# Optimization experiments

Measured on AMD Instinct MI355X. Metric: run time of the kernel, lower is better.

Reference implementation:

```python
import jax, jax.numpy as jnp
import numpy as np

N_NODES = 50000
N_EDGES = 1600000
IN_CH = 128
HID_CH = 128


def setup_inputs() -> dict:
    key = jax.random.key(0)
    ks = jax.random.split(key, 8)
    node_embed = jax.random.normal(ks[0], (N_NODES, IN_CH), dtype=jnp.float32)
    node_pos = jax.random.normal(ks[1], (N_NODES, 3), dtype=jnp.float32)
    edge_index = jax.random.randint(ks[2], (2, N_EDGES), 0, N_NODES, dtype=jnp.int64)
    # Linear weights stored as [in, out] so y = x @ W + b (matches torch x @ W.T + b)
    W_res = jax.random.normal(ks[3], (IN_CH, HID_CH), dtype=jnp.float32) / np.sqrt(IN_CH)
    W_msg = jax.random.normal(ks[4], (2 * IN_CH + 1, HID_CH), dtype=jnp.float32) / np.sqrt(2 * IN_CH + 1)
    b_msg = jax.random.normal(ks[5], (HID_CH,), dtype=jnp.float32) * 0.01
    W_upd = jax.random.normal(ks[6], (IN_CH + HID_CH, HID_CH), dtype=jnp.float32) / np.sqrt(IN_CH + HID_CH)
    b_upd = jax.random.normal(ks[7], (HID_CH,), dtype=jnp.float32) * 0.01
    return {"node_embed": node_embed, "node_pos": node_pos, "edge_index": edge_index,
            "W_res": W_res, "W_msg": W_msg, "b_msg": b_msg, "W_upd": W_upd, "b_upd": b_upd}


def reference(node_embed, node_pos, edge_index, W_res, W_msg, b_msg, W_upd, b_upd):
    row, col = edge_index[0], edge_index[1]
    # squared distance per edge: [E, 1]
    diff = node_pos[row] - node_pos[col]
    dist = jnp.sum(diff * diff, axis=1, keepdims=True)
    # message MLP on concat(src, tgt, dist): [E, 2*in+1] -> [E, hidden]
    msg_in = jnp.concatenate([node_embed[row], node_embed[col], dist], axis=-1)
    msg = jax.nn.relu(msg_in @ W_msg + b_msg)
    # scatter-sum messages into target nodes (index = col, as in original)
    aggr = jax.ops.segment_sum(msg, col, num_segments=N_NODES)
    upd_in = jnp.concatenate([node_embed, aggr], axis=-1)
    new_node_embed = node_embed @ W_res + jax.nn.relu(upd_in @ W_upd + b_upd)
    return new_node_embed
```

## Files before the change

### kernel.cpp

```cpp
#include <hip/hip_runtime.h>
#include <hip/hip_bf16.h>
#include <cstdint>


typedef __bf16 bf16x8 __attribute__((ext_vector_type(8)));
typedef float floatx4 __attribute__((ext_vector_type(4)));
typedef float floatx2 __attribute__((ext_vector_type(2)));
typedef unsigned int uintx4 __attribute__((ext_vector_type(4)));

#define NBINS 1024
#define BIN_CAP 2560
#define CAP_OUT 2816
#define CUR_STRIDE 32

__device__ __forceinline__ ushort f2bf(float f) {
  union { float f; uint i; } v; v.f = f;
  uint r = v.i + 0x7fff + ((v.i >> 16) & 1);
  return (ushort)(r >> 16);
}
__device__ __forceinline__ bf16x8 load_frag(const ushort* p) {
  uint4 v = *(const uint4*)p;
  return __builtin_bit_cast(bf16x8, v);
}
__device__ __forceinline__ floatx2 pmax0(floatx2 a) {
#if __has_builtin(__builtin_elementwise_max)
  return __builtin_elementwise_max(a, (floatx2)(0.f));
#else
  floatx2 r; r.x = fmaxf(a.x, 0.f); r.y = fmaxf(a.y, 0.f); return r;
#endif
}
__device__ __forceinline__ floatx2 cvtpk2(uint qu) {
#if __has_builtin(__builtin_amdgcn_cvt_pk_f32_fp8)
  return __builtin_amdgcn_cvt_pk_f32_fp8((int)qu, false);
#else
  floatx2 o = {__builtin_amdgcn_cvt_f32_fp8((int)qu, 0),
               __builtin_amdgcn_cvt_f32_fp8((int)qu, 1)};
  return o;
#endif
}

struct WSrc { const float* s[5]; };

__global__ __launch_bounds__(256) void k01_cast_bin(
    const float* __restrict__ embed, ushort* __restrict__ Eb, int n4, int nb_cast,
    WSrc ws, ushort* __restrict__ Wt,
    const int* __restrict__ ei, int E,
    uint* __restrict__ bin_cursor, uint* __restrict__ binned, int bb)
{
  __shared__ uint hist[NBINS];
  __shared__ uint sbase[NBINS];
  __shared__ uint lcur[NBINS];

  if ((int)blockIdx.x >= bb) {
    int cb = blockIdx.x - bb;
    if (cb < nb_cast) {
      int i = cb * 256 + threadIdx.x;
      if (i < n4) {
        float4 v = ((const float4*)embed)[i];
        ushort4 o;
        o.x = f2bf(v.x); o.y = f2bf(v.y); o.z = f2bf(v.z); o.w = f2bf(v.w);
        ((ushort4*)Eb)[i] = o;
      }
      return;
    }
    int wb = cb - nb_cast;
    const float* s = ws.s[wb];
    ushort* d = Wt + wb * 16384;
    for (int i = threadIdx.x; i < 16384; i += 256) {
      int k = i >> 7, n = i & 127;
      d[n * 128 + k] = f2bf(s[i]);
    }
    return;
  }

  const int t = threadIdx.x;
#pragma unroll
  for (int k = 0; k < NBINS / 256; ++k) hist[t + k * 256] = 0;
  __syncthreads();

  const int e0 = blockIdx.x * 2048 + t * 8;
  int rr[8], cc[8];
  bool any = (e0 < E);
  if (any) {
    int4 r0 = ((const int4*)(ei + e0))[0];
    int4 r1 = ((const int4*)(ei + e0))[1];
    int4 c0 = ((const int4*)(ei + E + e0))[0];
    int4 c1 = ((const int4*)(ei + E + e0))[1];
    rr[0]=r0.x; rr[1]=r0.y; rr[2]=r0.z; rr[3]=r0.w;
    rr[4]=r1.x; rr[5]=r1.y; rr[6]=r1.z; rr[7]=r1.w;
    cc[0]=c0.x; cc[1]=c0.y; cc[2]=c0.z; cc[3]=c0.w;
    cc[4]=c1.x; cc[5]=c1.y; cc[6]=c1.z; cc[7]=c1.w;
#pragma unroll
    for (int j = 0; j < 8; ++j) {
      if (e0 + j < E) atomicAdd(&hist[cc[j] >> 6], 1u);
    }
  }
  __syncthreads();
#pragma unroll
  for (int k = 0; k < NBINS / 256; ++k) {
    int b2 = t + k * 256;
    uint h = hist[b2];
    sbase[b2] = h ? atomicAdd(bin_cursor + b2 * CUR_STRIDE, h) : 0u;
    lcur[b2] = 0;
  }
  __syncthreads();
  if (any) {
#pragma unroll
    for (int j = 0; j < 8; ++j) {
      if (e0 + j < E) {
        int b = cc[j] >> 6;
        uint ofs = atomicAdd(&lcur[b], 1u);
        uint idx = sbase[b] + ofs;
        if (idx < BIN_CAP)
          binned[(size_t)b * BIN_CAP + idx] = ((uint)cc[j] << 16) | (uint)rr[j];
      }
    }
  }
}

__global__ __launch_bounds__(256) void k2_proj_sort(
    const ushort* __restrict__ Ab, int M, int rt,
    const ushort* __restrict__ W1t, const ushort* __restrict__ W2t,
    const float* __restrict__ b_msg, const float* __restrict__ pos,
    unsigned char* __restrict__ P1, ushort* __restrict__ P2b,
    const uint* __restrict__ bin_cursor, const uint* __restrict__ binned,
    uint* __restrict__ sorted, int* __restrict__ nstart, int* __restrict__ ncnt)
{
  __shared__ ushort sdist[BIN_CAP];
  __shared__ uint   srt[CAP_OUT];
  __shared__ float  spos[64 * 3];
  __shared__ uint   h[64], st[64], lc[64];
  __shared__ uint   stot;

  if ((int)blockIdx.x >= rt) {
    const int bin = blockIdx.x - rt;
    const int col0 = bin * 64;
    const int tid = threadIdx.x;
    const int cnt = (int)min(bin_cursor[bin * CUR_STRIDE], (uint)BIN_CAP);
    const uint* src = binned + (size_t)bin * BIN_CAP;
    const int ncol = min(64, M - col0);

    if (tid < 64) { h[tid] = 0; lc[tid] = 0; }
    for (int i = tid; i < ncol * 3; i += 256) spos[i] = pos[(size_t)col0 * 3 + i];
    __syncthreads();

    for (int i = tid; i < cnt; i += 256) {
      uint rc = src[i];
      uint row = rc & 0xffffu, cl = (rc >> 16) & 63u;
      float dx = spos[cl * 3 + 0] - pos[(size_t)row * 3 + 0];
      float dy = spos[cl * 3 + 1] - pos[(size_t)row * 3 + 1];
      float dz = spos[cl * 3 + 2] - pos[(size_t)row * 3 + 2];
      sdist[i] = f2bf(dx * dx + dy * dy + dz * dz);
      atomicAdd(&h[cl], 1u);
    }
    __syncthreads();

    if (tid == 0) {
      uint s = 0;
      for (int c = 0; c < 64; ++c) { st[c] = s; s += (h[c] + 3u) & ~3u; }
      stot = s;
    }
    __syncthreads();

    for (int i = tid; i < cnt; i += 256) {
      uint rc = src[i];
      uint row = rc & 0xffffu, cl = (rc >> 16) & 63u;
      uint p = st[cl] + atomicAdd(&lc[cl], 1u);
      if (p < CAP_OUT) srt[p] = (row << 16) | (uint)sdist[i];
    }
    __syncthreads();

    uint tot = min(stot, (uint)CAP_OUT);
    for (int i = tid; i < (int)tot; i += 256)
      sorted[(size_t)bin * CAP_OUT + i] = srt[i];
    if (tid < 64 && tid < ncol) {
      nstart[col0 + tid] = bin * CAP_OUT + (int)st[tid];
      ncnt[col0 + tid] = (int)h[tid];
    }
    return;
  }

  const int wv = threadIdx.x >> 6, lane = threadIdx.x & 63;
  const int q = lane >> 4, lr = lane & 15;
  const int m0 = blockIdx.x * 32;
  const int n0 = wv * 32;

  const ushort* Wt2[2] = {W1t, W2t};
  bf16x8 bfr[2][2][4];
#pragma unroll
  for (int ws = 0; ws < 2; ++ws)
#pragma unroll
    for (int nt = 0; nt < 2; ++nt) {
      int colc = n0 + nt * 16 + lr;
#pragma unroll
      for (int kc = 0; kc < 4; ++kc)
        bfr[ws][nt][kc] = load_frag(Wt2[ws] + colc * 128 + kc * 32 + q * 8);
    }

  floatx4 z = {0.f, 0.f, 0.f, 0.f};
  floatx4 acc[2][2][2];
#pragma unroll
  for (int ws = 0; ws < 2; ++ws)
#pragma unroll
    for (int mt = 0; mt < 2; ++mt)
#pragma unroll
      for (int nt = 0; nt < 2; ++nt) acc[ws][mt][nt] = z;

  const int r0 = min(m0 + lr, M - 1);
  const int r1 = min(m0 + 16 + lr, M - 1);
#pragma unroll
  for (int kc = 0; kc < 4; ++kc) {
    bf16x8 a0 = load_frag(Ab + (size_t)r0 * 128 + kc * 32 + q * 8);
    bf16x8 a1 = load_frag(Ab + (size_t)r1 * 128 + kc * 32 + q * 8);
#pragma unroll
    for (int ws = 0; ws < 2; ++ws)
#pragma unroll
      for (int nt = 0; nt < 2; ++nt) {
        acc[ws][0][nt] = __builtin_amdgcn_mfma_f32_16x16x32_bf16(a0, bfr[ws][nt][kc], acc[ws][0][nt], 0, 0, 0);
        acc[ws][1][nt] = __builtin_amdgcn_mfma_f32_16x16x32_bf16(a1, bfr[ws][nt][kc], acc[ws][1][nt], 0, 0, 0);
      }
  }

#pragma unroll
  for (int nt = 0; nt < 2; ++nt) {
    int colc = n0 + nt * 16 + lr;
    float bias = b_msg[colc];
#pragma unroll
    for (int mt = 0; mt < 2; ++mt)
#pragma unroll
      for (int i = 0; i < 4; ++i) {
        int r = m0 + mt * 16 + q * 4 + i;
        if (r < M) {
          int p8 = __builtin_amdgcn_cvt_pk_fp8_f32(acc[0][mt][nt][i], 0.f, 0, false);
          P1[(size_t)r * 128 + colc] = (unsigned char)(p8 & 0xff);
          P2b[(size_t)r * 128 + colc] = f2bf(acc[1][mt][nt][i] + bias);
        }
      }
  }
}

__global__ __launch_bounds__(256) void aggregate(const int* __restrict__ ncnt,
                                                 const int* __restrict__ nstart,
                                                 const uint* __restrict__ sorted,
                                                 const unsigned char* __restrict__ P1,
                                                 const ushort* __restrict__ P2b,
                                                 const float* __restrict__ wd,
                                                 ushort* __restrict__ aggr, int M)
{
  const int lane = threadIdx.x & 63;
  const int ch = lane * 2;
  const int wid = blockIdx.x * 4 + (threadIdx.x >> 6);
  const int nw = gridDim.x * 4;

  float2 wl = *(const float2*)(wd + ch);
  floatx2 wv = {wl.x, wl.y};

  for (int n = wid; n < M; n += nw) {
    uint p2u = *(const uint*)(P2b + (size_t)n * 128 + ch);
    floatx2 p2 = {__int_as_float((int)(p2u << 16)),
                  __int_as_float((int)(p2u & 0xffff0000u))};

    const int cnt = ncnt[n];
    const uint* base = sorted + nstart[n];

    floatx2 accA = {0.f, 0.f}, accB = {0.f, 0.f};

    auto edge = [&](uint rec, floatx2& acc) {
      float d = __int_as_float((int)(rec << 16));
      uint off = ((rec >> 9) & 0x007fff80u) | (uint)ch;
      uint qu = (uint)*(const ushort*)(P1 + off);
#if __has_builtin(__builtin_elementwise_fma)
      floatx2 u = __builtin_elementwise_fma((floatx2)(d), wv, p2);
#else
      floatx2 u = (floatx2)(d) * wv + p2;
#endif
      floatx2 t = cvtpk2(qu) + u;
      acc += pmax0(t);
    };

    int i = 0;
    for (; i + 8 <= cnt; i += 8) {
      uintx4 ra = __builtin_nontemporal_load((const uintx4*)(base + i));
      uintx4 rb = __builtin_nontemporal_load((const uintx4*)(base + i + 4));
      edge(ra.x, accA); edge(ra.y, accB); edge(ra.z, accA); edge(ra.w, accB);
      edge(rb.x, accA); edge(rb.y, accB); edge(rb.z, accA); edge(rb.w, accB);
    }
    for (; i < cnt; ++i) edge(base[i], accA);

    floatx2 acc = accA + accB;
    uint o = (uint)f2bf(acc.x) | ((uint)f2bf(acc.y) << 16);
    *(uint*)(aggr + (size_t)n * 128 + ch) = o;
  }
}

__global__ __launch_bounds__(256) void gemm_upd_mfma(
    const ushort* __restrict__ Eb, const ushort* __restrict__ Gb, int M,
    const ushort* __restrict__ Wu1t, const ushort* __restrict__ Wu2t,
    const ushort* __restrict__ Wrt, const float* __restrict__ b_upd,
    float* __restrict__ out)
{
  const int wv = threadIdx.x >> 6, lane = threadIdx.x & 63;
  const int q = lane >> 4, lr = lane & 15;
  const int m0 = blockIdx.x * 32;
  const int n0 = wv * 32;

  bf16x8 b1[2][4], b2[2][4], br[2][4];
#pragma unroll
  for (int nt = 0; nt < 2; ++nt) {
    int colc = n0 + nt * 16 + lr;
#pragma unroll
    for (int kc = 0; kc < 4; ++kc) {
      b1[nt][kc] = load_frag(Wu1t + colc * 128 + kc * 32 + q * 8);
      b2[nt][kc] = load_frag(Wu2t + colc * 128 + kc * 32 + q * 8);
      br[nt][kc] = load_frag(Wrt  + colc * 128 + kc * 32 + q * 8);
    }
  }

  floatx4 z = {0.f, 0.f, 0.f, 0.f};
  floatx4 acc_u[2][2], acc_r[2][2];
#pragma unroll
  for (int mt = 0; mt < 2; ++mt)
#pragma unroll
    for (int nt = 0; nt < 2; ++nt) { acc_u[mt][nt] = z; acc_r[mt][nt] = z; }

  const int r0 = min(m0 + lr, M - 1);
  const int r1 = min(m0 + 16 + lr, M - 1);
#pragma unroll
  for (int kc = 0; kc < 4; ++kc) {
    bf16x8 ae0 = load_frag(Eb + (size_t)r0 * 128 + kc * 32 + q * 8);
    bf16x8 ae1 = load_frag(Eb + (size_t)r1 * 128 + kc * 32 + q * 8);
    bf16x8 ag0 = load_frag(Gb + (size_t)r0 * 128 + kc * 32 + q * 8);
    bf16x8 ag1 = load_frag(Gb + (size_t)r1 * 128 + kc * 32 + q * 8);
#pragma unroll
    for (int nt = 0; nt < 2; ++nt) {
      acc_u[0][nt] = __builtin_amdgcn_mfma_f32_16x16x32_bf16(ae0, b1[nt][kc], acc_u[0][nt], 0, 0, 0);
      acc_u[1][nt] = __builtin_amdgcn_mfma_f32_16x16x32_bf16(ae1, b1[nt][kc], acc_u[1][nt], 0, 0, 0);
      acc_u[0][nt] = __builtin_amdgcn_mfma_f32_16x16x32_bf16(ag0, b2[nt][kc], acc_u[0][nt], 0, 0, 0);
      acc_u[1][nt] = __builtin_amdgcn_mfma_f32_16x16x32_bf16(ag1, b2[nt][kc], acc_u[1][nt], 0, 0, 0);
      acc_r[0][nt] = __builtin_amdgcn_mfma_f32_16x16x32_bf16(ae0, br[nt][kc], acc_r[0][nt], 0, 0, 0);
      acc_r[1][nt] = __builtin_amdgcn_mfma_f32_16x16x32_bf16(ae1, br[nt][kc], acc_r[1][nt], 0, 0, 0);
    }
  }

#pragma unroll
  for (int nt = 0; nt < 2; ++nt) {
    int colc = n0 + nt * 16 + lr;
    float bias = b_upd[colc];
#pragma unroll
    for (int mt = 0; mt < 2; ++mt)
#pragma unroll
      for (int i = 0; i < 4; ++i) {
        int r = m0 + mt * 16 + q * 4 + i;
        if (r < M)
          out[(size_t)r * 128 + colc] = acc_r[mt][nt][i] + fmaxf(acc_u[mt][nt][i] + bias, 0.f);
      }
  }
}

extern "C" void kernel_launch(void* const* d_in, const int* in_sizes, int n_in,
                              void* d_out, int out_size, void* d_ws, size_t ws_size,
                              hipStream_t stream)
{
  const float* embed = (const float*)d_in[0];
  const float* pos   = (const float*)d_in[1];
  const int*   ei    = (const int*)d_in[2];
  const float* W_res = (const float*)d_in[3];
  const float* W_msg = (const float*)d_in[4];
  const float* b_msg = (const float*)d_in[5];
  const float* W_upd = (const float*)d_in[6];
  const float* b_upd = (const float*)d_in[7];
  float* out = (float*)d_out;

  const int M = in_sizes[0] / 128;
  const int E = in_sizes[2] / 2;

  ushort* Eb = (ushort*)d_ws;
  unsigned char* P1f8 = (unsigned char*)(Eb + (size_t)M * 128);
  ushort* P2b = (ushort*)(P1f8 + (size_t)M * 128);
  ushort* Gb  = P2b + (size_t)M * 128;
  ushort* Wt  = Gb  + (size_t)M * 128;
  uint*   binned = (uint*)(Wt + 5 * 16384);
  uint*   sorted = binned + (size_t)NBINS * BIN_CAP;
  int*    nstart = (int*)(sorted + (size_t)NBINS * CAP_OUT);
  int*    ncnt   = nstart + M;
  uint*   bin_cursor = (uint*)(ncnt + M);

  (void)hipMemsetAsync(bin_cursor, 0, (size_t)NBINS * CUR_STRIDE * sizeof(uint), stream);

  WSrc wsrc;
  wsrc.s[0] = W_msg;
  wsrc.s[1] = W_msg + 128 * 128;
  wsrc.s[2] = W_res;
  wsrc.s[3] = W_upd;
  wsrc.s[4] = W_upd + 128 * 128;

  int n4 = M * 128 / 4;
  int nb_cast = (n4 + 255) / 256;
  int bb = (E + 2047) / 2048;
  k01_cast_bin<<<bb + nb_cast + 5, 256, 0, stream>>>(
      embed, Eb, n4, nb_cast, wsrc, Wt, ei, E, bin_cursor, binned, bb);

  int rt = (M + 31) / 32;
  int nbin2 = (M + 63) / 64;
  k2_proj_sort<<<rt + nbin2, 256, 0, stream>>>(
      Eb, M, rt, Wt, Wt + 16384, b_msg, pos, P1f8, P2b,
      bin_cursor, binned, sorted, nstart, ncnt);

  int ab = min((M + 3) / 4, 2048);
  aggregate<<<ab, 256, 0, stream>>>(ncnt, nstart, sorted, P1f8, P2b,
                                    W_msg + 256 * 128, Gb, M);

  gemm_upd_mfma<<<rt, 256, 0, stream>>>(Eb, Gb, M, Wt + 3 * 16384, Wt + 4 * 16384,
                                        Wt + 2 * 16384, b_upd, out);
}
```

Measured before the change: 271.4 us.

## Use coarse 512-node super-bins and scatter sorted edges directly to global

Edge binning drops from 1024 bins of 64 target nodes to at most 128 super-bins of 512 nodes. This cuts per-block global cursor atomics and LDS histogram work in the binning kernel. The sort stage now does a separate histogram pass, an LDS prefix scan and a direct scatter to the global sorted buffer, unrolled 8 edges per thread, instead of staging in LDS. In exchange only about 98 sort blocks handle roughly 16k edges each, which risks a long serial tail and uncoalesced global writes.

```diff
diff --git a/kernel.cpp b/kernel.cpp
--- a/kernel.cpp
+++ b/kernel.cpp
@@ -8,9 +8,10 @@
 typedef float floatx2 __attribute__((ext_vector_type(2)));
 typedef unsigned int uintx4 __attribute__((ext_vector_type(4)));
 
-#define NBINS 1024
-#define BIN_CAP 2560
-#define CAP_OUT 2816
+#define SBINS 128
+#define SBIN_SHIFT 9
+#define BIN_CAP 17408
+#define CAP_OUT 19456
 #define CUR_STRIDE 32
 
 __device__ __forceinline__ ushort f2bf(float f) {
@@ -47,9 +48,9 @@
     const int* __restrict__ ei, int E,
     uint* __restrict__ bin_cursor, uint* __restrict__ binned, int bb)
 {
-  __shared__ uint hist[NBINS];
-  __shared__ uint sbase[NBINS];
-  __shared__ uint lcur[NBINS];
+  __shared__ uint hist[SBINS];
+  __shared__ uint sbase[SBINS];
+  __shared__ uint lcur[SBINS];
 
   if ((int)blockIdx.x >= bb) {
     int cb = blockIdx.x - bb;
@@ -74,8 +75,7 @@
   }
 
   const int t = threadIdx.x;
-#pragma unroll
-  for (int k = 0; k < NBINS / 256; ++k) hist[t + k * 256] = 0;
+  if (t < SBINS) hist[t] = 0;
   __syncthreads();
 
   const int e0 = blockIdx.x * 2048 + t * 8;
@@ -92,23 +92,21 @@
     cc[4]=c1.x; cc[5]=c1.y; cc[6]=c1.z; cc[7]=c1.w;
 #pragma unroll
     for (int j = 0; j < 8; ++j) {
-      if (e0 + j < E) atomicAdd(&hist[cc[j] >> 6], 1u);
+      if (e0 + j < E) atomicAdd(&hist[cc[j] >> SBIN_SHIFT], 1u);
     }
   }
   __syncthreads();
-#pragma unroll
-  for (int k = 0; k < NBINS / 256; ++k) {
-    int b2 = t + k * 256;
-    uint h = hist[b2];
-    sbase[b2] = h ? atomicAdd(bin_cursor + b2 * CUR_STRIDE, h) : 0u;
-    lcur[b2] = 0;
+  if (t < SBINS) {
+    uint h = hist[t];
+    sbase[t] = h ? atomicAdd(bin_cursor + t * CUR_STRIDE, h) : 0u;
+    lcur[t] = 0;
   }
   __syncthreads();
   if (any) {
 #pragma unroll
     for (int j = 0; j < 8; ++j) {
       if (e0 + j < E) {
-        int b = cc[j] >> 6;
+        int b = cc[j] >> SBIN_SHIFT;
         uint ofs = atomicAdd(&lcur[b], 1u);
         uint idx = sbase[b] + ofs;
         if (idx < BIN_CAP)
@@ -126,56 +124,81 @@
     const uint* __restrict__ bin_cursor, const uint* __restrict__ binned,
     uint* __restrict__ sorted, int* __restrict__ nstart, int* __restrict__ ncnt)
 {
-  __shared__ ushort sdist[BIN_CAP];
-  __shared__ uint   srt[CAP_OUT];
-  __shared__ float  spos[64 * 3];
-  __shared__ uint   h[64], st[64], lc[64];
-  __shared__ uint   stot;
+  __shared__ uint  hist[512], st[512], lcur[512];
+  __shared__ uint  part[256];
+  __shared__ float spos[512 * 3];
 
   if ((int)blockIdx.x >= rt) {
     const int bin = blockIdx.x - rt;
-    const int col0 = bin * 64;
+    const int col0 = bin << SBIN_SHIFT;
     const int tid = threadIdx.x;
     const int cnt = (int)min(bin_cursor[bin * CUR_STRIDE], (uint)BIN_CAP);
     const uint* src = binned + (size_t)bin * BIN_CAP;
-    const int ncol = min(64, M - col0);
-
-    if (tid < 64) { h[tid] = 0; lc[tid] = 0; }
+    const int ncol = min(512, M - col0);
+
+    for (int i = tid; i < 512; i += 256) { hist[i] = 0; lcur[i] = 0; }
     for (int i = tid; i < ncol * 3; i += 256) spos[i] = pos[(size_t)col0 * 3 + i];
     __syncthreads();
 
-    for (int i = tid; i < cnt; i += 256) {
+    for (int i = tid; i < cnt; i += 256)
+      atomicAdd(&hist[(src[i] >> 16) & 511u], 1u);
+    __syncthreads();
+
+    {
+      uint a = hist[2 * tid], b = hist[2 * tid + 1];
+      part[tid] = ((a + 3u) & ~3u) + ((b + 3u) & ~3u);
+    }
+    __syncthreads();
+    if (tid == 0) {
+      uint run = 0;
+      for (int k = 0; k < 256; ++k) { uint tmp = part[k]; part[k] = run; run += tmp; }
+    }
+    __syncthreads();
+    {
+      uint a = hist[2 * tid];
+      st[2 * tid] = part[tid];
+      st[2 * tid + 1] = part[tid] + ((a + 3u) & ~3u);
+    }
+    __syncthreads();
+
+    const size_t obase = (size_t)bin * CAP_OUT;
+    int i = tid;
+    for (; i + 1792 < cnt; i += 2048) {
+      uint rc[8]; float dd[8];
+#pragma unroll
+      for (int j = 0; j < 8; ++j) rc[j] = src[i + j * 256];
+#pragma unroll
+      for (int j = 0; j < 8; ++j) {
+        uint row = rc[j] & 0xffffu;
+        uint cl  = (rc[j] >> 16) & 511u;
+        float dx = spos[cl * 3 + 0] - pos[(size_t)row * 3 + 0];
+        float dy = spos[cl * 3 + 1] - pos[(size_t)row * 3 + 1];
+        float dz = spos[cl * 3 + 2] - pos[(size_t)row * 3 + 2];
+        dd[j] = dx * dx + dy * dy + dz * dz;
+      }
+#pragma unroll
+      for (int j = 0; j < 8; ++j) {
+        uint cl = (rc[j] >> 16) & 511u;
+        uint p = st[cl] + atomicAdd(&lcur[cl], 1u);
+        sorted[obase + p] = (rc[j] << 16) | (uint)f2bf(dd[j]);
+      }
+    }
+    for (; i < cnt; i += 256) {
       uint rc = src[i];
-      uint row = rc & 0xffffu, cl = (rc >> 16) & 63u;
+      uint row = rc & 0xffffu;
+      uint cl  = (rc >> 16) & 511u;
       float dx = spos[cl * 3 + 0] - pos[(size_t)row * 3 + 0];
       float dy = spos[cl * 3 + 1] - pos[(size_t)row * 3 + 1];
       float dz = spos[cl * 3 + 2] - pos[(size_t)row * 3 + 2];
-      sdist[i] = f2bf(dx * dx + dy * dy + dz * dz);
-      atomicAdd(&h[cl], 1u);
-    }
-    __syncthreads();
-
-    if (tid == 0) {
-      uint s = 0;
-      for (int c = 0; c < 64; ++c) { st[c] = s; s += (h[c] + 3u) & ~3u; }
-      stot = s;
-    }
-    __syncthreads();
-
-    for (int i = tid; i < cnt; i += 256) {
-      uint rc = src[i];
-      uint row = rc & 0xffffu, cl = (rc >> 16) & 63u;
-      uint p = st[cl] + atomicAdd(&lc[cl], 1u);
-      if (p < CAP_OUT) srt[p] = (row << 16) | (uint)sdist[i];
-    }
-    __syncthreads();
-
-    uint tot = min(stot, (uint)CAP_OUT);
-    for (int i = tid; i < (int)tot; i += 256)
-      sorted[(size_t)bin * CAP_OUT + i] = srt[i];
-    if (tid < 64 && tid < ncol) {
-      nstart[col0 + tid] = bin * CAP_OUT + (int)st[tid];
-      ncnt[col0 + tid] = (int)h[tid];
+      float d = dx * dx + dy * dy + dz * dz;
+      uint p = st[cl] + atomicAdd(&lcur[cl], 1u);
+      sorted[obase + p] = (rc << 16) | (uint)f2bf(d);
+    }
+    __syncthreads();
+
+    for (int c = tid; c < ncol; c += 256) {
+      nstart[col0 + c] = (int)(obase + st[c]);
+      ncnt[col0 + c] = (int)hist[c];
     }
     return;
   }
@@ -380,12 +403,12 @@
   ushort* Gb  = P2b + (size_t)M * 128;
   ushort* Wt  = Gb  + (size_t)M * 128;
   uint*   binned = (uint*)(Wt + 5 * 16384);
-  uint*   sorted = binned + (size_t)NBINS * BIN_CAP;
-  int*    nstart = (int*)(sorted + (size_t)NBINS * CAP_OUT);
+  uint*   sorted = binned + (size_t)SBINS * BIN_CAP;
+  int*    nstart = (int*)(sorted + (size_t)SBINS * CAP_OUT);
   int*    ncnt   = nstart + M;
   uint*   bin_cursor = (uint*)(ncnt + M);
 
-  (void)hipMemsetAsync(bin_cursor, 0, (size_t)NBINS * CUR_STRIDE * sizeof(uint), stream);
+  (void)hipMemsetAsync(bin_cursor, 0, (size_t)SBINS * CUR_STRIDE * sizeof(uint), stream);
 
   WSrc wsrc;
   wsrc.s[0] = W_msg;
@@ -401,8 +424,8 @@
       embed, Eb, n4, nb_cast, wsrc, Wt, ei, E, bin_cursor, binned, bb);
 
   int rt = (M + 31) / 32;
-  int nbin2 = (M + 63) / 64;
-  k2_proj_sort<<<rt + nbin2, 256, 0, stream>>>(
+  int nsb = (M + 511) >> SBIN_SHIFT;
+  k2_proj_sort<<<rt + nsb, 256, 0, stream>>>(
       Eb, M, rt, Wt, Wt + 16384, b_msg, pos, P1f8, P2b,
       bin_cursor, binned, sorted, nstart, ncnt);
 
```

Measured after the change: 278.2 us. +2.5%, slower.
